# Performance work log

Measured on AMD Instinct MI355X. Metric: run time of the kernel, lower is better.

Reference implementation:

```python
import jax, jax.numpy as jnp
import numpy as np

D_MODEL = 1024
D_HIDDEN = 1024  # must equal D_MODEL (SSM adds C(h) [.,d_model] + D(x) [.,d_hidden])
B, T = 8, 1022   # T chosen so T+2 == D_MODEL, required by the `x @ x_res` batched matmul


def setup_inputs() -> dict:
    key = jax.random.key(0)
    ks = jax.random.split(key, 12)
    def w(k, shape, s=0.02):
        return jax.random.normal(k, shape, jnp.float32) * s
    return {
        "x": jax.random.normal(ks[0], (B, T, D_MODEL), jnp.float32),
        "w1": w(ks[1], (D_MODEL, D_MODEL)),
        "w2": w(ks[2], (D_MODEL, D_MODEL)),
        "w_last": w(ks[3], (D_MODEL, D_MODEL)),
        "conv_w": w(ks[4], (D_MODEL, 1, 3), 0.1),  # depthwise conv kernel [out, in/groups, k]
        "conv_b": jnp.zeros((D_MODEL,), jnp.float32),
        "A": jnp.abs(jax.random.normal(ks[5], (D_HIDDEN,), jnp.float32)) + 0.1,  # positive -> stable decay
        "wB": w(ks[6], (D_MODEL, D_HIDDEN)), "bB": jnp.zeros((D_HIDDEN,), jnp.float32),
        "wC": w(ks[7], (D_HIDDEN, D_MODEL)), "bC": jnp.zeros((D_MODEL,), jnp.float32),
        "wD": w(ks[8], (D_MODEL, D_HIDDEN)), "bD": jnp.zeros((D_HIDDEN,), jnp.float32),
        "wdelta": w(ks[9], (D_MODEL, D_HIDDEN)), "bdelta": jnp.zeros((D_HIDDEN,), jnp.float32),
    }


def _scan_combine(l, r):
    # linear recurrence h_t = a_t * h_{t-1} + b_t as an associative op
    aL, bL = l
    aR, bR = r
    return (aL * aR, aR * bL + bR)


def reference(x, w1, w2, w_last, conv_w, conv_b, A, wB, bB, wC, bC, wD, bD, wdelta, bdelta):
    x = x @ w1  # [B,T,D]
    # depthwise causal-ish conv, padding=2 on both sides (as in torch code) -> length T+2
    xc = jnp.transpose(x, (0, 2, 1))  # [B,D,T]
    xc = jax.lax.conv_general_dilated(
        xc, conv_w, window_strides=(1,), padding=[(2, 2)],
        dimension_numbers=("NCH", "OIH", "NCH"), feature_group_count=D_MODEL)
    xc = xc + conv_b[None, :, None]
    x = jnp.transpose(xc, (0, 2, 1))  # [B, T+2, D]
    x = jax.nn.silu(x)
    # --- SSM selective scan ---
    x_delta = jax.nn.softplus(x @ wdelta + bdelta)      # [B,T+2,Dh]
    A_bar = jnp.exp(-x_delta * A)                       # [B,T+2,Dh]
    B_x = x @ wB + bB                                   # [B,T+2,Dh]
    _, h = jax.lax.associative_scan(_scan_combine, (A_bar, B_x), axis=1)
    ssm_out = (h @ wC + bC) + (x @ wD + bD)             # [B,T+2,D] (Dh == D)
    # --- gating + output ---
    x_res = jax.nn.silu(ssm_out @ w2)                   # [B,T+2,D]
    z = jnp.matmul(ssm_out, x_res)                      # batched matmul: valid since D == T+2
    out = z @ w_last                                    # [B, T+2, D]
    return out
```

## Files before the change

### kernel.cpp

```cpp
#include <hip/hip_runtime.h>

typedef __bf16 bf16x8 __attribute__((ext_vector_type(8)));
typedef float  f32x4  __attribute__((ext_vector_type(4)));
typedef unsigned short u16x8 __attribute__((ext_vector_type(8)));

__device__ __forceinline__ float b2f(unsigned short u) {
  union { float f; unsigned int i; } v; v.i = ((unsigned int)u) << 16; return v.f;
}
__device__ __forceinline__ unsigned short f2b(float f) {
  union { float f; unsigned int i; } v; v.f = f;
  unsigned int r = v.i + 0x7fffu + ((v.i >> 16) & 1u);
  return (unsigned short)(r >> 16);
}

__device__ __forceinline__ void async_copy16(const unsigned short* g, unsigned short* l) {
  __builtin_amdgcn_global_load_lds(
      (__attribute__((address_space(1))) void*)g,
      (__attribute__((address_space(3))) void*)l, 16, 0, 0);
}

__global__ void k_prep_w(const float* w0, const float* w1_, const float* w2_,
                         const float* w3_, const float* w4_, const float* w5_,
                         const float* w6_, unsigned short* dst) {
  const float* srcs[7] = {w0, w1_, w2_, w3_, w4_, w5_, w6_};
  const float* src = srcs[blockIdx.z];
  unsigned short* d = dst + ((size_t)blockIdx.z << 20);
  __shared__ float tile[32][33];
  const int bn = blockIdx.x << 5, bk = blockIdx.y << 5;
  const int tx = threadIdx.x, ty = threadIdx.y;
#pragma unroll
  for (int i = 0; i < 4; ++i)
    tile[ty + i * 8][tx] = src[(size_t)(bk + ty + i * 8) * 1024 + bn + tx];
  __syncthreads();
#pragma unroll
  for (int i = 0; i < 4; ++i)
    d[(size_t)(bn + ty + i * 8) * 1024 + bk + tx] = f2b(tile[tx][ty + i * 8]);
}

__global__ void k_prep_cw(const float* __restrict__ cw, float* __restrict__ cwT) {
  const int idx = blockIdx.x * 256 + threadIdx.x;
  const int d = idx & 1023, j = idx >> 10;
  cwT[idx] = cw[d * 3 + j];
}

__global__ void k_cast_x(const float* __restrict__ x, unsigned short* __restrict__ xb) {
  const size_t i = ((size_t)blockIdx.x * 256 + threadIdx.x) << 2;
  const int d = (int)(i & 1023);
  const int row = (int)(i >> 10);
  const int t = row & 1023, b = row >> 10;
  float4 v = make_float4(0.f, 0.f, 0.f, 0.f);
  if (t < 1022) v = *(const float4*)&x[((size_t)(b * 1022 + t) << 10) + d];
  ushort4 o;
  o.x = f2b(v.x); o.y = f2b(v.y); o.z = f2b(v.z); o.w = f2b(v.w);
  *(ushort4*)&xb[i] = o;
}

__global__ void k_conv_silu(const unsigned short* __restrict__ x1, const float* __restrict__ cwT,
                            const float* __restrict__ cb, unsigned short* __restrict__ xs) {
  const int gid = blockIdx.x * 256 + threadIdx.x;
  const int row = gid >> 7;
  const int d0 = (gid & 127) << 3;
  const int b = row >> 10, i = row & 1023;
  float acc[8];
  {
    float4 c0 = *(const float4*)&cb[d0], c1 = *(const float4*)&cb[d0 + 4];
    acc[0] = c0.x; acc[1] = c0.y; acc[2] = c0.z; acc[3] = c0.w;
    acc[4] = c1.x; acc[5] = c1.y; acc[6] = c1.z; acc[7] = c1.w;
  }
#pragma unroll
  for (int j = 0; j < 3; ++j) {
    const int t = i + j - 2;
    if (t >= 0) {
      u16x8 v = *(const u16x8*)&x1[((size_t)(b * 1024 + t) << 10) + d0];
      float4 w0 = *(const float4*)&cwT[j * 1024 + d0];
      float4 w1 = *(const float4*)&cwT[j * 1024 + d0 + 4];
      acc[0] += b2f(v[0]) * w0.x; acc[1] += b2f(v[1]) * w0.y;
      acc[2] += b2f(v[2]) * w0.z; acc[3] += b2f(v[3]) * w0.w;
      acc[4] += b2f(v[4]) * w1.x; acc[5] += b2f(v[5]) * w1.y;
      acc[6] += b2f(v[6]) * w1.z; acc[7] += b2f(v[7]) * w1.w;
    }
  }
  u16x8 o;
#pragma unroll
  for (int k = 0; k < 8; ++k) {
    float s = acc[k] / (1.f + expf(-acc[k]));
    o[k] = f2b(s);
  }
  *(u16x8*)&xs[((size_t)row << 10) + d0] = o;
}

__global__ void k_scan1(const float* __restrict__ Abar, const unsigned short* __restrict__ Bx,
                        float* __restrict__ cA, float* __restrict__ cB) {
  const int g = blockIdx.x * 256 + threadIdx.x;
  const int d = g & 1023, bc = g >> 10;
  const int b = bc >> 4, c = bc & 15;
  size_t base = ((size_t)(b * 1024 + c * 64) << 10) + d;
  float aA = 1.f, aB = 0.f;
  for (int t = 0; t < 64; ++t) {
    float a = Abar[base], bx = b2f(Bx[base]);
    aA *= a; aB = a * aB + bx; base += 1024;
  }
  cA[g] = aA; cB[g] = aB;
}
__global__ void k_scan2(const float* __restrict__ cA, const float* __restrict__ cB,
                        float* __restrict__ carry) {
  const int g = blockIdx.x * 256 + threadIdx.x;
  const int d = g & 1023, b = g >> 10;
  float a[16], bb[16];
#pragma unroll
  for (int c = 0; c < 16; ++c) {
    const int idx = ((b * 16 + c) << 10) + d;
    a[c] = cA[idx]; bb[c] = cB[idx];
  }
  float sB = 0.f;
#pragma unroll
  for (int c = 0; c < 16; ++c) {
    carry[((b * 16 + c) << 10) + d] = sB;
    sB = a[c] * sB + bb[c];
  }
}
__global__ void k_scan3(const float* __restrict__ Abar, const unsigned short* __restrict__ Bx,
                        const float* __restrict__ carry, unsigned short* __restrict__ hb) {
  const int g = blockIdx.x * 256 + threadIdx.x;
  const int d = g & 1023, bc = g >> 10;
  const int b = bc >> 4, c = bc & 15;
  size_t base = ((size_t)(b * 1024 + c * 64) << 10) + d;
  float h = carry[g];
  for (int t = 0; t < 64; ++t) {
    float a = Abar[base], bx = b2f(Bx[base]);
    h = a * h + bx;
    hb[base] = f2b(h);
    base += 1024;
  }
}

__global__ void k_transpose_xres(const unsigned short* __restrict__ src,
                                 unsigned short* __restrict__ dst) {
  __shared__ unsigned short tile[32][33];
  const int b = blockIdx.z;
  const int bx = blockIdx.x << 5, by = blockIdx.y << 5;
  const int tx = threadIdx.x, ty = threadIdx.y;
  const unsigned short* s = src + ((size_t)b << 20);
  unsigned short* d = dst + ((size_t)b << 20);
#pragma unroll
  for (int i = 0; i < 4; ++i)
    tile[ty + i * 8][tx] = s[(size_t)(by + ty + i * 8) * 1024 + bx + tx];
  __syncthreads();
#pragma unroll
  for (int i = 0; i < 4; ++i)
    d[(size_t)(bx + ty + i * 8) * 1024 + by + tx] = tile[tx][ty + i * 8];
}

template <int EPI, bool BATCHB>
__global__ __launch_bounds__(256)
void k_gemm(const unsigned short* __restrict__ A, const unsigned short* __restrict__ Bt,
            void* __restrict__ outp, const float* __restrict__ aux1,
            const void* __restrict__ aux2,
            void* __restrict__ out2, void* __restrict__ out3,
            const float* __restrict__ aux3, const float* __restrict__ aux4) {
  __shared__ unsigned short As[2][128 * 64];
  __shared__ unsigned short Bs[2][128 * 64];
  const int tid = threadIdx.x;

  const int nxb = gridDim.x;
  const int nwg = nxb * gridDim.y;
  int lin = blockIdx.y * nxb + blockIdx.x;
  lin = (lin & 7) * (nwg >> 3) + (lin >> 3);
  const int CH = nxb << 3;
  const int grp = lin / CH, idx = lin % CH;
  const int m0 = ((grp << 3) + (idx & 7)) << 7;
  const int n0 = (idx >> 3) << 7;

  const int wid = tid >> 6, l = tid & 63;
  const int wr = ((wid >> 1) << 6);
  const int wc = ((wid & 1) << 6);
  const int lr = l & 15, kg = l >> 4;
  const unsigned short* Bp = BATCHB ? Bt + ((size_t)(m0 >> 10) << 20) : Bt;

  f32x4 acc[4][4];
#pragma unroll
  for (int i = 0; i < 4; ++i)
#pragma unroll
    for (int j = 0; j < 4; ++j) acc[i][j] = (f32x4){0.f, 0.f, 0.f, 0.f};

  const int frow = tid >> 3;
  const int fchunk = (tid & 7) ^ (frow & 7);
  const size_t aBase = (size_t)(m0 + frow) * 1024 + (fchunk << 3);
  const size_t bBase = (size_t)(n0 + frow) * 1024 + (fchunk << 3);

#define STAGE(buf, k0)                                                          \
  {                                                                             \
    _Pragma("unroll")                                                           \
    for (int it = 0; it < 4; ++it)                                              \
      async_copy16(A + aBase + (size_t)(it * 32) * 1024 + (k0),                 \
                   &As[buf][(tid << 3) + it * 2048]);                           \
    _Pragma("unroll")                                                           \
    for (int it = 0; it < 4; ++it)                                              \
      async_copy16(Bp + bBase + (size_t)(it * 32) * 1024 + (k0),                \
                   &Bs[buf][(tid << 3) + it * 2048]);                           \
  }

  STAGE(0, 0);
  STAGE(1, 64);

#pragma unroll
  for (int t = 0; t < 16; ++t) {
    const int cur = t & 1;
    if (t < 15) asm volatile("s_waitcnt vmcnt(8)" ::: "memory");
    else        asm volatile("s_waitcnt vmcnt(0)" ::: "memory");
    __builtin_amdgcn_s_barrier();
    __builtin_amdgcn_sched_barrier(0);
#pragma unroll
    for (int ks = 0; ks < 2; ++ks) {
      bf16x8 aF[4], bF[4];
#pragma unroll
      for (int mi = 0; mi < 4; ++mi) {
        const int row = wr + mi * 16 + lr;
        aF[mi] = *(const bf16x8*)&As[cur][(row << 6) + (((ks * 4 + kg) ^ (lr & 7)) << 3)];
      }
#pragma unroll
      for (int ni = 0; ni < 4; ++ni) {
        const int row = wc + ni * 16 + lr;
        bF[ni] = *(const bf16x8*)&Bs[cur][(row << 6) + (((ks * 4 + kg) ^ (lr & 7)) << 3)];
      }
#pragma unroll
      for (int mi = 0; mi < 4; ++mi)
#pragma unroll
        for (int ni = 0; ni < 4; ++ni)
          acc[mi][ni] = __builtin_amdgcn_mfma_f32_16x16x32_bf16(aF[mi], bF[ni], acc[mi][ni], 0, 0, 0);
    }
    asm volatile("s_waitcnt lgkmcnt(0)" ::: "memory");
    __builtin_amdgcn_s_barrier();
    __builtin_amdgcn_sched_barrier(0);
    if (t + 2 < 16) STAGE(cur, (t + 2) * 64);
  }
#undef STAGE

#pragma unroll
  for (int mi = 0; mi < 4; ++mi) {
    const int rowb = m0 + wr + mi * 16 + (kg << 2);
#pragma unroll
    for (int ni = 0; ni < 4; ++ni) {
      const int col = n0 + wc + ni * 16 + lr;
#pragma unroll
      for (int r = 0; r < 4; ++r) {
        const int row = rowb + r;
        const size_t idx2 = ((size_t)row << 10) + col;
        float v = acc[mi][ni][r];
        if (EPI == 0) {
          ((unsigned short*)outp)[idx2] = f2b(v);
        } else if (EPI == 3) {
          v += aux1[col] + b2f(((const unsigned short*)aux2)[idx2]);
          ((unsigned short*)outp)[idx2] = f2b(v);
        } else if (EPI == 4) {
          ((unsigned short*)outp)[idx2] = f2b(v / (1.f + expf(-v)));
        } else if (EPI == 5) {
          ((float*)outp)[idx2] = v;
        } else {
          const int seg = n0 >> 10;
          const int c1 = col & 1023;
          const size_t idx3 = ((size_t)row << 10) + c1;
          if (seg == 0) {
            float v2 = v + aux1[c1];
            float sp = (v2 > 20.f) ? v2 : log1pf(expf(v2));
            ((float*)outp)[idx3] = expf(-sp * ((const float*)aux2)[c1]);
          } else if (seg == 1) {
            ((unsigned short*)out2)[idx3] = f2b(v + aux3[c1]);
          } else {
            ((unsigned short*)out3)[idx3] = f2b(v + aux4[c1]);
          }
        }
      }
    }
  }
}

extern "C" void kernel_launch(void* const* d_in, const int* in_sizes, int n_in,
                              void* d_out, int out_size, void* d_ws, size_t ws_size,
                              hipStream_t stream) {
  const float* x      = (const float*)d_in[0];
  const float* w1     = (const float*)d_in[1];
  const float* w2     = (const float*)d_in[2];
  const float* w_last = (const float*)d_in[3];
  const float* conv_w = (const float*)d_in[4];
  const float* conv_b = (const float*)d_in[5];
  const float* Avec   = (const float*)d_in[6];
  const float* wB     = (const float*)d_in[7];
  const float* bB     = (const float*)d_in[8];
  const float* wC     = (const float*)d_in[9];
  const float* bC     = (const float*)d_in[10];
  const float* wD     = (const float*)d_in[11];
  const float* bD     = (const float*)d_in[12];
  const float* wdelta = (const float*)d_in[13];
  const float* bdelta = (const float*)d_in[14];

  char* ws = (char*)d_ws;
  const size_t MB = 1ull << 20;
  const size_t NW = 1ull << 20;
  unsigned short* wT   = (unsigned short*)(ws);
  unsigned short* xb   = (unsigned short*)(ws + 14 * MB);
  unsigned short* x1   = (unsigned short*)(ws + 30 * MB);
  unsigned short* xs   = (unsigned short*)(ws + 46 * MB);
  float*          Abar = (float*)(ws + 62 * MB);
  unsigned short* Bx   = (unsigned short*)(ws + 94 * MB);
  unsigned short* xD   = (unsigned short*)(ws + 110 * MB);
  float*          cA   = (float*)(ws + 126 * MB);
  float*          cB   = (float*)(ws + 126 * MB + 512 * 1024);
  float*          carry= (float*)(ws + 127 * MB);
  float*          cwT  = (float*)(ws + 127 * MB + 512 * 1024);
  unsigned short* hb    = xs;
  unsigned short* ssm   = xb;
  unsigned short* xres  = x1;
  unsigned short* xresT = (unsigned short*)(ws + 62 * MB);
  unsigned short* z     = (unsigned short*)(ws + 78 * MB);

  dim3 bT(32, 8);
  dim3 gG(8, 64);
  dim3 gF(24, 64);

  k_prep_w<<<dim3(32, 32, 7), bT, 0, stream>>>(w1, wdelta, wB, wD, wC, w2, w_last, wT);
  k_prep_cw<<<12, 256, 0, stream>>>(conv_w, cwT);
  k_cast_x<<<8192, 256, 0, stream>>>(x, xb);
  k_gemm<0, false><<<gG, 256, 0, stream>>>(xb, wT + 0 * NW, x1, nullptr, nullptr,
                                           nullptr, nullptr, nullptr, nullptr);
  k_conv_silu<<<4096, 256, 0, stream>>>(x1, cwT, conv_b, xs);
  k_gemm<6, false><<<gF, 256, 0, stream>>>(xs, wT + 1 * NW, Abar, bdelta, (const void*)Avec,
                                           Bx, xD, bB, bD);
  k_scan1<<<512, 256, 0, stream>>>(Abar, Bx, cA, cB);
  k_scan2<<<32, 256, 0, stream>>>(cA, cB, carry);
  k_scan3<<<512, 256, 0, stream>>>(Abar, Bx, carry, hb);
  k_gemm<3, false><<<gG, 256, 0, stream>>>(hb, wT + 4 * NW, ssm, bC, (const void*)xD,
                                           nullptr, nullptr, nullptr, nullptr);
  k_gemm<4, false><<<gG, 256, 0, stream>>>(ssm, wT + 5 * NW, xres, nullptr, nullptr,
                                           nullptr, nullptr, nullptr, nullptr);
  k_transpose_xres<<<dim3(32, 32, 8), bT, 0, stream>>>(xres, xresT);
  k_gemm<0, true><<<gG, 256, 0, stream>>>(ssm, xresT, z, nullptr, nullptr,
                                          nullptr, nullptr, nullptr, nullptr);
  k_gemm<5, false><<<gG, 256, 0, stream>>>(z, wT + 6 * NW, (float*)d_out, nullptr, nullptr,
                                           nullptr, nullptr, nullptr, nullptr);
}
```

Baseline: 292.6 us.

## Split fused triple-output GEMM into three launches and streamline GEMM address math

The fused GEMM that computed delta, B and D projections in one wide launch (24x64 grid with a per-segment epilogue branch) is split into three separate 8x64 launches with specialized epilogues. The inner loop now uses incrementing global pointers and precomputed swizzled LDS byte offsets instead of recomputing indices. It also raises wave priority around the MFMA block with s_setprio. The aim is less address arithmetic and simpler epilogues, at the cost of two extra launches and losing one large grid that filled the GPU better.

```diff
diff --git a/kernel.cpp b/kernel.cpp
--- a/kernel.cpp
+++ b/kernel.cpp
@@ -155,9 +155,7 @@
 __global__ __launch_bounds__(256)
 void k_gemm(const unsigned short* __restrict__ A, const unsigned short* __restrict__ Bt,
             void* __restrict__ outp, const float* __restrict__ aux1,
-            const void* __restrict__ aux2,
-            void* __restrict__ out2, void* __restrict__ out3,
-            const float* __restrict__ aux3, const float* __restrict__ aux4) {
+            const void* __restrict__ aux2) {
   __shared__ unsigned short As[2][128 * 64];
   __shared__ unsigned short Bs[2][128 * 64];
   const int tid = threadIdx.x;
@@ -185,23 +183,36 @@
 
   const int frow = tid >> 3;
   const int fchunk = (tid & 7) ^ (frow & 7);
-  const size_t aBase = (size_t)(m0 + frow) * 1024 + (fchunk << 3);
-  const size_t bBase = (size_t)(n0 + frow) * 1024 + (fchunk << 3);
-
-#define STAGE(buf, k0)                                                          \
+  const unsigned short* ga[4];
+  const unsigned short* gb[4];
+#pragma unroll
+  for (int it = 0; it < 4; ++it) {
+    ga[it] = A  + (size_t)(m0 + frow + it * 32) * 1024 + (fchunk << 3);
+    gb[it] = Bp + (size_t)(n0 + frow + it * 32) * 1024 + (fchunk << 3);
+  }
+
+#define STAGE(buf)                                                              \
   {                                                                             \
     _Pragma("unroll")                                                           \
     for (int it = 0; it < 4; ++it)                                              \
-      async_copy16(A + aBase + (size_t)(it * 32) * 1024 + (k0),                 \
-                   &As[buf][(tid << 3) + it * 2048]);                           \
+      async_copy16(ga[it], &As[buf][(tid << 3) + it * 2048]);                   \
     _Pragma("unroll")                                                           \
     for (int it = 0; it < 4; ++it)                                              \
-      async_copy16(Bp + bBase + (size_t)(it * 32) * 1024 + (k0),                \
-                   &Bs[buf][(tid << 3) + it * 2048]);                           \
-  }
-
-  STAGE(0, 0);
-  STAGE(1, 64);
+      async_copy16(gb[it], &Bs[buf][(tid << 3) + it * 2048]);                   \
+    _Pragma("unroll")                                                           \
+    for (int it = 0; it < 4; ++it) { ga[it] += 64; gb[it] += 64; }              \
+  }
+
+  const int c0 = kg ^ (lr & 7);
+  const int aOff0 = ((wr + lr) << 7) + (c0 << 4);
+  const int aOff1 = aOff0 ^ 64;
+  const int bOff0 = ((wc + lr) << 7) + (c0 << 4);
+  const int bOff1 = bOff0 ^ 64;
+  const char* AsB = (const char*)&As[0][0];
+  const char* BsB = (const char*)&Bs[0][0];
+
+  STAGE(0);
+  STAGE(1);
 
 #pragma unroll
   for (int t = 0; t < 16; ++t) {
@@ -210,29 +221,38 @@
     else        asm volatile("s_waitcnt vmcnt(0)" ::: "memory");
     __builtin_amdgcn_s_barrier();
     __builtin_amdgcn_sched_barrier(0);
-#pragma unroll
-    for (int ks = 0; ks < 2; ++ks) {
+    __builtin_amdgcn_s_setprio(1);
+    const char* pa = AsB + (cur << 14);
+    const char* pb = BsB + (cur << 14);
+    {
       bf16x8 aF[4], bF[4];
 #pragma unroll
-      for (int mi = 0; mi < 4; ++mi) {
-        const int row = wr + mi * 16 + lr;
-        aF[mi] = *(const bf16x8*)&As[cur][(row << 6) + (((ks * 4 + kg) ^ (lr & 7)) << 3)];
-      }
-#pragma unroll
-      for (int ni = 0; ni < 4; ++ni) {
-        const int row = wc + ni * 16 + lr;
-        bF[ni] = *(const bf16x8*)&Bs[cur][(row << 6) + (((ks * 4 + kg) ^ (lr & 7)) << 3)];
-      }
+      for (int mi = 0; mi < 4; ++mi) aF[mi] = *(const bf16x8*)(pa + aOff0 + mi * 2048);
+#pragma unroll
+      for (int ni = 0; ni < 4; ++ni) bF[ni] = *(const bf16x8*)(pb + bOff0 + ni * 2048);
 #pragma unroll
       for (int mi = 0; mi < 4; ++mi)
 #pragma unroll
         for (int ni = 0; ni < 4; ++ni)
           acc[mi][ni] = __builtin_amdgcn_mfma_f32_16x16x32_bf16(aF[mi], bF[ni], acc[mi][ni], 0, 0, 0);
     }
+    {
+      bf16x8 aF[4], bF[4];
+#pragma unroll
+      for (int mi = 0; mi < 4; ++mi) aF[mi] = *(const bf16x8*)(pa + aOff1 + mi * 2048);
+#pragma unroll
+      for (int ni = 0; ni < 4; ++ni) bF[ni] = *(const bf16x8*)(pb + bOff1 + ni * 2048);
+#pragma unroll
+      for (int mi = 0; mi < 4; ++mi)
+#pragma unroll
+        for (int ni = 0; ni < 4; ++ni)
+          acc[mi][ni] = __builtin_amdgcn_mfma_f32_16x16x32_bf16(aF[mi], bF[ni], acc[mi][ni], 0, 0, 0);
+    }
+    __builtin_amdgcn_s_setprio(0);
     asm volatile("s_waitcnt lgkmcnt(0)" ::: "memory");
     __builtin_amdgcn_s_barrier();
     __builtin_amdgcn_sched_barrier(0);
-    if (t + 2 < 16) STAGE(cur, (t + 2) * 64);
+    if (t + 2 < 16) STAGE(cur);
   }
 #undef STAGE
 
@@ -249,26 +269,19 @@
         float v = acc[mi][ni][r];
         if (EPI == 0) {
           ((unsigned short*)outp)[idx2] = f2b(v);
+        } else if (EPI == 1) {
+          float v2 = v + aux1[col];
+          float sp = (v2 > 20.f) ? v2 : log1pf(expf(v2));
+          ((float*)outp)[idx2] = expf(-sp * ((const float*)aux2)[col]);
+        } else if (EPI == 2) {
+          ((unsigned short*)outp)[idx2] = f2b(v + aux1[col]);
         } else if (EPI == 3) {
           v += aux1[col] + b2f(((const unsigned short*)aux2)[idx2]);
           ((unsigned short*)outp)[idx2] = f2b(v);
         } else if (EPI == 4) {
           ((unsigned short*)outp)[idx2] = f2b(v / (1.f + expf(-v)));
-        } else if (EPI == 5) {
+        } else {
           ((float*)outp)[idx2] = v;
-        } else {
-          const int seg = n0 >> 10;
-          const int c1 = col & 1023;
-          const size_t idx3 = ((size_t)row << 10) + c1;
-          if (seg == 0) {
-            float v2 = v + aux1[c1];
-            float sp = (v2 > 20.f) ? v2 : log1pf(expf(v2));
-            ((float*)outp)[idx3] = expf(-sp * ((const float*)aux2)[c1]);
-          } else if (seg == 1) {
-            ((unsigned short*)out2)[idx3] = f2b(v + aux3[c1]);
-          } else {
-            ((unsigned short*)out3)[idx3] = f2b(v + aux4[c1]);
-          }
         }
       }
     }
@@ -316,26 +329,21 @@
 
   dim3 bT(32, 8);
   dim3 gG(8, 64);
-  dim3 gF(24, 64);
 
   k_prep_w<<<dim3(32, 32, 7), bT, 0, stream>>>(w1, wdelta, wB, wD, wC, w2, w_last, wT);
   k_prep_cw<<<12, 256, 0, stream>>>(conv_w, cwT);
   k_cast_x<<<8192, 256, 0, stream>>>(x, xb);
-  k_gemm<0, false><<<gG, 256, 0, stream>>>(xb, wT + 0 * NW, x1, nullptr, nullptr,
-                                           nullptr, nullptr, nullptr, nullptr);
+  k_gemm<0, false><<<gG, 256, 0, stream>>>(xb, wT + 0 * NW, x1, nullptr, nullptr);
   k_conv_silu<<<4096, 256, 0, stream>>>(x1, cwT, conv_b, xs);
-  k_gemm<6, false><<<gF, 256, 0, stream>>>(xs, wT + 1 * NW, Abar, bdelta, (const void*)Avec,
-                                           Bx, xD, bB, bD);
+  k_gemm<1, false><<<gG, 256, 0, stream>>>(xs, wT + 1 * NW, Abar, bdelta, (const void*)Avec);
+  k_gemm<2, false><<<gG, 256, 0, stream>>>(xs, wT + 2 * NW, Bx, bB, nullptr);
+  k_gemm<2, false><<<gG, 256, 0, stream>>>(xs, wT + 3 * NW, xD, bD, nullptr);
   k_scan1<<<512, 256, 0, stream>>>(Abar, Bx, cA, cB);
   k_scan2<<<32, 256, 0, stream>>>(cA, cB, carry);
   k_scan3<<<512, 256, 0, stream>>>(Abar, Bx, carry, hb);
-  k_gemm<3, false><<<gG, 256, 0, stream>>>(hb, wT + 4 * NW, ssm, bC, (const void*)xD,
-                                           nullptr, nullptr, nullptr, nullptr);
-  k_gemm<4, false><<<gG, 256, 0, stream>>>(ssm, wT + 5 * NW, xres, nullptr, nullptr,
-                                           nullptr, nullptr, nullptr, nullptr);
+  k_gemm<3, false><<<gG, 256, 0, stream>>>(hb, wT + 4 * NW, ssm, bC, (const void*)xD);
+  k_gemm<4, false><<<gG, 256, 0, stream>>>(ssm, wT + 5 * NW, xres, nullptr, nullptr);
   k_transpose_xres<<<dim3(32, 32, 8), bT, 0, stream>>>(xres, xresT);
-  k_gemm<0, true><<<gG, 256, 0, stream>>>(ssm, xresT, z, nullptr, nullptr,
-                                          nullptr, nullptr, nullptr, nullptr);
-  k_gemm<5, false><<<gG, 256, 0, stream>>>(z, wT + 6 * NW, (float*)d_out, nullptr, nullptr,
-                                           nullptr, nullptr, nullptr, nullptr);
-}
+  k_gemm<0, true><<<gG, 256, 0, stream>>>(ssm, xresT, z, nullptr, nullptr);
+  k_gemm<5, false><<<gG, 256, 0, stream>>>(z, wT + 6 * NW, (float*)d_out, nullptr, nullptr);
+}
```

Result: faster. 273.2 us (-6.6%).
